# Kernel tuning notes

Measured on AMD Instinct MI355X. Metric: run time of the kernel, lower is better.

## Reference

```python
import jax, jax.numpy as jnp
import numpy as np

N_NODES = 50000
N_EDGES = 800000
IN_FEAT = 128
HEADS = 4
UNITS = 16
LEAKY_ALPHA = 0.2  # tf.nn.leaky_relu default


def setup_inputs() -> dict:
    key = jax.random.key(0)
    k1, k2, k3, k4, k5 = jax.random.split(key, 5)
    x = jax.random.normal(k1, (N_NODES, IN_FEAT), dtype=jnp.float32)
    edge_index = jax.random.randint(k2, (N_EDGES, 2), 0, N_NODES, dtype=jnp.int32)
    # Dense kernel (glorot-ish scaling), no bias (use_bias=False)
    W = jax.random.normal(k3, (IN_FEAT, HEADS * UNITS), dtype=jnp.float32) * (1.0 / np.sqrt(IN_FEAT))
    glorot = np.sqrt(2.0 / (1 + UNITS)).astype(np.float32)
    att_w1 = jax.random.normal(k4, (HEADS, 1, UNITS), dtype=jnp.float32) * glorot
    att_w2 = jax.random.normal(k5, (HEADS, 1, UNITS), dtype=jnp.float32) * glorot
    return {"x": x, "edge_index": edge_index, "W": W, "att_w1": att_w1, "att_w2": att_w2}


def reference(x, edge_index, W, att_w1, att_w2):
    n_nodes = x.shape[0]
    h = x @ W  # [N, H*U]
    snd_idx = edge_index[:, 0]
    rcv_idx = edge_index[:, 1]
    # gather per-edge features, split into heads -> [H, E, U]
    sender = h[snd_idx].reshape(-1, HEADS, UNITS).transpose(1, 0, 2)
    receiver = h[rcv_idx].reshape(-1, HEADS, UNITS).transpose(1, 0, 2)
    # per-edge, per-head attention logits [H, E]
    att = jnp.sum(att_w1 * sender, axis=-1) + jnp.sum(att_w2 * receiver, axis=-1)
    att = jnp.where(att > 0, att, LEAKY_ALPHA * att)
    # segment softmax over receiver neighborhoods, per head
    seg_max = jax.vmap(lambda a: jax.ops.segment_max(a, rcv_idx, num_segments=n_nodes))(att)  # [H, N]
    e = jnp.exp(att - seg_max[:, rcv_idx])
    denom = jax.vmap(lambda a: jax.ops.segment_sum(a, rcv_idx, num_segments=n_nodes))(e)  # [H, N]
    alpha = e / denom[:, rcv_idx]  # [H, E]
    # weighted scatter-sum of sender features -> [H, N, U]
    out = jax.vmap(lambda v: jax.ops.segment_sum(v, rcv_idx, num_segments=n_nodes))(sender * alpha[:, :, None])
    # concat heads -> [N, H*U]; activation is None (identity)
    return out.transpose(1, 0, 2).reshape(n_nodes, HEADS * UNITS)
```

## Files before the change

kernel.cpp:

```cpp
#include <hip/hip_runtime.h>
#include <math.h>

#define N_NODES 50000
#define N_EDGES 800000
#define IN_FEAT 128
#define HEADS   4
#define UNITS   16
#define OUTF    64
#define LEAKY   0.2f

#define NB      196
#define BCAP    5120
#define CAP     64
#define GEMM_BLKS 782
#define A_BLOCKS  196
#define EPB     16

typedef __attribute__((ext_vector_type(8))) short bf16x8;
typedef __attribute__((ext_vector_type(4))) float f32x4;

__device__ __forceinline__ unsigned short f2bf(float f) {
    unsigned u = __float_as_uint(f);
    unsigned r = u + 0x7FFFu + ((u >> 16) & 1u);
    return (unsigned short)(r >> 16);
}
__device__ __forceinline__ float bf2f(unsigned short b) {
    return __uint_as_float(((unsigned)b) << 16);
}

union SharedU {
    struct { unsigned short wt[64 * 136]; } g;
    struct { unsigned stage[4096]; int hist[256], cur[256], adj[256], wsum[4]; } a;
};

__global__ __launch_bounds__(256) void prep(const float* __restrict__ W,
                                            const float* __restrict__ w1,
                                            const float* __restrict__ w2,
                                            unsigned short* __restrict__ Wt_g,
                                            unsigned short* __restrict__ Wea_g,
                                            int* __restrict__ bucket_cnt) {
    int idx = blockIdx.x * 256 + threadIdx.x;
    if (idx < NB) bucket_cnt[idx] = 0;
    if (idx < IN_FEAT * OUTF) {
        int k = idx >> 6, c = idx & 63;
        Wt_g[c * IN_FEAT + k] = f2bf(W[idx]);
    }
    if (idx < IN_FEAT * HEADS) {
        int k = idx >> 2, hd = idx & 3;
        float s1 = 0.f, s2 = 0.f;
        #pragma unroll
        for (int u = 0; u < UNITS; ++u) {
            float wv = W[k * OUTF + hd * UNITS + u];
            s1 += wv * w1[hd * UNITS + u];
            s2 += wv * w2[hd * UNITS + u];
        }
        unsigned short h1 = f2bf(s1), h2 = f2bf(s2);
        unsigned short l1 = f2bf(s1 - bf2f(h1)), l2 = f2bf(s2 - bf2f(h2));
        Wea_g[(hd)      * IN_FEAT + k] = h1;
        Wea_g[(4 + hd)  * IN_FEAT + k] = h2;
        Wea_g[(8 + hd)  * IN_FEAT + k] = l1;
        Wea_g[(12 + hd) * IN_FEAT + k] = l2;
    }
}

__global__ __launch_bounds__(256, 8) void fused_gemm_bucketA(const float* __restrict__ x,
                                                             const unsigned short* __restrict__ Wt_g,
                                                             const unsigned short* __restrict__ Wea_g,
                                                             const int2* __restrict__ ei,
                                                             unsigned short* __restrict__ hg,
                                                             float* __restrict__ a1,
                                                             float* __restrict__ a2,
                                                             int* __restrict__ bucket_cnt,
                                                             unsigned* __restrict__ buckets) {
    __shared__ SharedU sh;
    const int t = threadIdx.x;
    const int lane = t & 63, wv = t >> 6;

    if (blockIdx.x >= GEMM_BLKS) {
        const int e0 = (blockIdx.x - GEMM_BLKS) * 4096;
        sh.a.hist[t] = 0;
        __syncthreads();

        unsigned pk[EPB]; int bk[EPB];
        #pragma unroll
        for (int j = 0; j < EPB; ++j) {
            int e = e0 + t + j * 256;
            if (e < N_EDGES) {
                int2 ed = ei[e];
                pk[j] = ((unsigned)ed.x << 16) | (unsigned)ed.y;
                bk[j] = ed.y >> 8;
                atomicAdd(&sh.a.hist[bk[j]], 1);
            } else bk[j] = -1;
        }
        __syncthreads();
        const int v = sh.a.hist[t];
        int inc = v;
        #pragma unroll
        for (int off = 1; off < 64; off <<= 1) {
            int u = __shfl_up(inc, off, 64);
            if (lane >= off) inc += u;
        }
        if (lane == 63) sh.a.wsum[wv] = inc;
        __syncthreads();
        const int s0 = sh.a.wsum[0], s1 = sh.a.wsum[1], s2 = sh.a.wsum[2];
        const int wo = (wv > 0 ? s0 : 0) + (wv > 1 ? s1 : 0) + (wv > 2 ? s2 : 0);
        const int excl = wo + inc - v;
        sh.a.cur[t] = excl;
        if (t < NB) {
            int g0 = atomicAdd(&bucket_cnt[t], v);
            sh.a.adj[t] = g0 - excl;
        }
        __syncthreads();
        #pragma unroll
        for (int j = 0; j < EPB; ++j) {
            if (bk[j] >= 0) {
                int p = atomicAdd(&sh.a.cur[bk[j]], 1);
                sh.a.stage[p] = pk[j];
            }
        }
        __syncthreads();
        const int total = min(4096, N_EDGES - e0);
        for (int i = t; i < total; i += 256) {
            unsigned vv = sh.a.stage[i];
            int b = (vv >> 8) & 255;
            buckets[(size_t)(b * BCAP + sh.a.adj[b] + i)] = vv;
        }
        return;
    }

    const int node0 = blockIdx.x * 64;
    unsigned short* wt = sh.g.wt;

    {
        const ushort4* Wt4 = (const ushort4*)Wt_g;
        #pragma unroll
        for (int it = 0; it < 8; ++it) {
            int idx = t + 256 * it;
            int c = idx >> 5, u = idx & 31;
            *(ushort4*)&wt[c * 136 + u * 4] = Wt4[idx];
        }
    }
    __syncthreads();

    const int m = lane & 15, quad = lane >> 4;
    const int n0 = wv * 16;
    const int arow = min(node0 + n0 + m, N_NODES - 1);
    const float* xr = x + (size_t)arow * IN_FEAT;

    f32x4 acc[4] = {{0,0,0,0},{0,0,0,0},{0,0,0,0},{0,0,0,0}};
    f32x4 acca   = {0,0,0,0};
    #pragma unroll
    for (int kc = 0; kc < 4; ++kc) {
        float4 v0 = *(const float4*)(xr + kc * 32 + quad * 8);
        float4 v1 = *(const float4*)(xr + kc * 32 + quad * 8 + 4);
        bf16x8 af;
        af[0] = (short)f2bf(v0.x); af[1] = (short)f2bf(v0.y);
        af[2] = (short)f2bf(v0.z); af[3] = (short)f2bf(v0.w);
        af[4] = (short)f2bf(v1.x); af[5] = (short)f2bf(v1.y);
        af[6] = (short)f2bf(v1.z); af[7] = (short)f2bf(v1.w);
        #pragma unroll
        for (int ct = 0; ct < 4; ++ct) {
            bf16x8 bfr = *(bf16x8*)&wt[(ct * 16 + m) * 136 + kc * 32 + quad * 8];
            acc[ct] = __builtin_amdgcn_mfma_f32_16x16x32_bf16(af, bfr, acc[ct], 0, 0, 0);
        }
        bf16x8 waf = *(const bf16x8*)(Wea_g + (size_t)m * IN_FEAT + kc * 32 + quad * 8);
        acca = __builtin_amdgcn_mfma_f32_16x16x32_bf16(af, waf, acca, 0, 0, 0);
    }

    #pragma unroll
    for (int r = 0; r < 4; ++r) {
        float vres = acca[r] + __shfl_xor(acca[r], 8, 64);
        int node = node0 + n0 + quad * 4 + r;
        if (node < N_NODES) {
            if (m < 4)      a1[node * 4 + m]       = vres;
            else if (m < 8) a2[node * 4 + (m - 4)] = vres;
        }
    }

    __syncthreads();
    unsigned short* hl = sh.g.wt;
    #pragma unroll
    for (int ct = 0; ct < 4; ++ct)
        #pragma unroll
        for (int r = 0; r < 4; ++r)
            hl[(n0 + quad * 4 + r) * 72 + ct * 16 + m] = f2bf(acc[ct][r]);
    __syncthreads();
    #pragma unroll
    for (int it = 0; it < 2; ++it) {
        int u = t + 256 * it;
        int r = u >> 3, cg = u & 7;
        int node = node0 + r;
        if (node < N_NODES)
            *(uint4*)&hg[(size_t)node * OUTF + cg * 8] = *(uint4*)&hl[r * 72 + cg * 8];
    }
}

__global__ __launch_bounds__(1024) void bucketB(const unsigned* __restrict__ buckets,
                                                const int* __restrict__ bucket_cnt,
                                                unsigned short* __restrict__ csr,
                                                int* __restrict__ deg) {
    __shared__ unsigned short snds[BCAP];
    __shared__ int hist[256], cur[256], strt[256], wsum[4];
    const int b = blockIdx.x;
    const int t = threadIdx.x;
    const int cnt = bucket_cnt[b];
    if (t < 256) hist[t] = 0;
    __syncthreads();
    for (int i = t; i < cnt; i += 1024)
        atomicAdd(&hist[buckets[(size_t)b * BCAP + i] & 255], 1);
    __syncthreads();
    int v = 0, inc = 0;
    if (t < 256) {
        const int lane = t & 63, wvx = t >> 6;
        v = hist[t];
        inc = v;
        #pragma unroll
        for (int off = 1; off < 64; off <<= 1) {
            int u = __shfl_up(inc, off, 64);
            if (lane >= off) inc += u;
        }
        if (lane == 63) wsum[wvx] = inc;
    }
    __syncthreads();
    if (t < 256) {
        const int wvx = t >> 6;
        const int s0 = wsum[0], s1 = wsum[1], s2 = wsum[2];
        const int wo = (wvx > 0 ? s0 : 0) + (wvx > 1 ? s1 : 0) + (wvx > 2 ? s2 : 0);
        const int excl = wo + inc - v;
        strt[t] = excl;
        cur[t]  = excl;
        const int node = b * 256 + t;
        if (node < N_NODES) deg[node] = v;
    }
    __syncthreads();
    for (int i = t; i < cnt; i += 1024) {
        unsigned vv = buckets[(size_t)b * BCAP + i];
        int p = atomicAdd(&cur[vv & 255], 1);
        snds[p] = (unsigned short)(vv >> 16);
    }
    __syncthreads();
    for (int u = t; u < 256 * CAP; u += 1024) {
        const int loc = u >> 6, slot = u & (CAP - 1);
        const int d = hist[loc];
        const unsigned short val = (d > 0) ? snds[strt[loc] + min(slot, d - 1)] : 0;
        csr[(size_t)b * (256 * CAP) + u] = val;
    }
}

__global__ __launch_bounds__(256, 8) void gather_kernel(const int* __restrict__ deg,
                                                        const unsigned short* __restrict__ csr,
                                                        const float* __restrict__ a1,
                                                        const float* __restrict__ a2,
                                                        const unsigned short* __restrict__ h,
                                                        float* __restrict__ out) {
    const int wave = threadIdx.x >> 6;
    const int lane = threadIdx.x & 63;
    const int n = blockIdx.x * 4 + wave;
    if (n >= N_NODES) return;
    const int sv = csr[(size_t)n * CAP + lane];
    const int cn = min(deg[n], CAP);
    const int sub  = lane >> 3;
    const int li   = lane & 7;
    const int head = li >> 1;
    if (cn <= 0) {
        if (sub == 0) {
            *(float4*)(out + (size_t)n * OUTF + li * 8)     = make_float4(0.f, 0.f, 0.f, 0.f);
            *(float4*)(out + (size_t)n * OUTF + li * 8 + 4) = make_float4(0.f, 0.f, 0.f, 0.f);
        }
        return;
    }
    const float a2h = a2[n * 4 + head];
    const uint4* h4 = (const uint4*)h;

    float acc[8] = {0.f,0.f,0.f,0.f,0.f,0.f,0.f,0.f};
    float den = 0.f;

    for (int i0 = 0; i0 < cn; i0 += 16) {
        #pragma unroll
        for (int g = 0; g < 2; ++g) {
            int er = i0 + g * 8 + sub;
            int ec = min(er, cn - 1);
            int s = __shfl(sv, ec, 64);
            float t0 = a1[s * 4 + head] + a2h;
            t0 = t0 > 0.f ? t0 : LEAKY * t0;
            float e = (er < cn) ? __expf(t0) : 0.f;
            uint4 hv = h4[(unsigned)(s * 8 + li)];
            const unsigned hw[4] = {hv.x, hv.y, hv.z, hv.w};
            #pragma unroll
            for (int q = 0; q < 4; ++q) {
                acc[q*2+0] = fmaf(e, __uint_as_float(hw[q] << 16),         acc[q*2+0]);
                acc[q*2+1] = fmaf(e, __uint_as_float(hw[q] & 0xFFFF0000u), acc[q*2+1]);
            }
            den += e;
        }
    }

    #pragma unroll
    for (int off = 8; off <= 32; off <<= 1) {
        #pragma unroll
        for (int q = 0; q < 8; ++q) acc[q] += __shfl_xor(acc[q], off, 64);
        den += __shfl_xor(den, off, 64);
    }

    if (sub == 0) {
        float inv = 1.f / den;
        *(float4*)(out + (size_t)n * OUTF + li * 8) =
            make_float4(acc[0] * inv, acc[1] * inv, acc[2] * inv, acc[3] * inv);
        *(float4*)(out + (size_t)n * OUTF + li * 8 + 4) =
            make_float4(acc[4] * inv, acc[5] * inv, acc[6] * inv, acc[7] * inv);
    }
}

extern "C" void kernel_launch(void* const* d_in, const int* in_sizes, int n_in,
                              void* d_out, int out_size, void* d_ws, size_t ws_size,
                              hipStream_t stream) {
    const float* x  = (const float*)d_in[0];
    const int2*  ei = (const int2*)d_in[1];
    const float* W  = (const float*)d_in[2];
    const float* w1 = (const float*)d_in[3];
    const float* w2 = (const float*)d_in[4];
    float* out = (float*)d_out;

    unsigned short* h    = (unsigned short*)d_ws;
    float* a1            = (float*)(h + (size_t)N_NODES * OUTF);
    float* a2            = a1 + (size_t)N_NODES * HEADS;
    unsigned short* Wt_g = (unsigned short*)(a2 + (size_t)N_NODES * HEADS);
    unsigned short* Wea_g = Wt_g + IN_FEAT * OUTF;
    int*   bucket_cnt    = (int*)(Wea_g + IN_FEAT * 16);
    unsigned* buckets    = (unsigned*)(bucket_cnt + 256);
    unsigned short* csr  = (unsigned short*)(buckets + (size_t)NB * BCAP);
    int*   deg           = (int*)(csr + (size_t)NB * 256 * CAP);

    prep<<<32, 256, 0, stream>>>(W, w1, w2, Wt_g, Wea_g, bucket_cnt);
    fused_gemm_bucketA<<<GEMM_BLKS + A_BLOCKS, 256, 0, stream>>>(x, Wt_g, Wea_g, ei,
                                                                 h, a1, a2,
                                                                 bucket_cnt, buckets);
    bucketB<<<NB, 1024, 0, stream>>>(buckets, bucket_cnt, csr, deg);
    gather_kernel<<<(N_NODES + 3) / 4, 256, 0, stream>>>(deg, csr, a1, a2, h, out);
}
```

Measured before the change: 125.8 us.

## Replace CSR build and per-node gather with bucket-local LDS atomic aggregation

Shrinks the receiver buckets to 64 nodes each and removes the second bucketing pass, the padded CSR and the per-node gather kernel. A new kernel walks each bucket's edges and accumulates exp-weighted sender features and denominators into shared memory with float atomics, using a rotated column layout to spread bank conflicts, then normalizes and writes out. This drops one kernel launch and the CSR write and read traffic, and also removes the 64-neighbor cap. In exchange it relies on shared-memory atomic throughput, skips the max subtraction, and makes the summation order nondeterministic.

```diff
diff --git a/kernel.cpp b/kernel.cpp
--- a/kernel.cpp
+++ b/kernel.cpp
@@ -9,12 +9,12 @@
 #define OUTF    64
 #define LEAKY   0.2f
 
-#define NB      196
-#define BCAP    5120
-#define CAP     64
+#define NB      782
+#define NBP     1024
+#define BCAP    1280
 #define GEMM_BLKS 782
-#define A_BLOCKS  196
-#define EPB     16
+#define A_BLOCKS  391
+#define EPB     8
 
 typedef __attribute__((ext_vector_type(8))) short bf16x8;
 typedef __attribute__((ext_vector_type(4))) float f32x4;
@@ -30,7 +30,8 @@
 
 union SharedU {
     struct { unsigned short wt[64 * 136]; } g;
-    struct { unsigned stage[4096]; int hist[256], cur[256], adj[256], wsum[4]; } a;
+    struct { unsigned stage[2048]; int hist[NBP], cur[NBP];
+             short adj[NBP]; int wsum[4]; } a;
 };
 
 __global__ __launch_bounds__(256) void prep(const float* __restrict__ W,
@@ -40,7 +41,7 @@
                                             unsigned short* __restrict__ Wea_g,
                                             int* __restrict__ bucket_cnt) {
     int idx = blockIdx.x * 256 + threadIdx.x;
-    if (idx < NB) bucket_cnt[idx] = 0;
+    if (idx < NBP) bucket_cnt[idx] = 0;
     if (idx < IN_FEAT * OUTF) {
         int k = idx >> 6, c = idx & 63;
         Wt_g[c * IN_FEAT + k] = f2bf(W[idx]);
@@ -77,8 +78,9 @@
     const int lane = t & 63, wv = t >> 6;
 
     if (blockIdx.x >= GEMM_BLKS) {
-        const int e0 = (blockIdx.x - GEMM_BLKS) * 4096;
-        sh.a.hist[t] = 0;
+        const int e0 = (blockIdx.x - GEMM_BLKS) * 2048;
+        #pragma unroll
+        for (int j = 0; j < 4; ++j) sh.a.hist[t + 256 * j] = 0;
         __syncthreads();
 
         unsigned pk[EPB]; int bk[EPB];
@@ -88,13 +90,15 @@
             if (e < N_EDGES) {
                 int2 ed = ei[e];
                 pk[j] = ((unsigned)ed.x << 16) | (unsigned)ed.y;
-                bk[j] = ed.y >> 8;
+                bk[j] = ed.y >> 6;
                 atomicAdd(&sh.a.hist[bk[j]], 1);
             } else bk[j] = -1;
         }
         __syncthreads();
-        const int v = sh.a.hist[t];
-        int inc = v;
+        const int h0 = sh.a.hist[4 * t + 0], h1 = sh.a.hist[4 * t + 1],
+                  h2 = sh.a.hist[4 * t + 2], h3 = sh.a.hist[4 * t + 3];
+        const int lsum = h0 + h1 + h2 + h3;
+        int inc = lsum;
         #pragma unroll
         for (int off = 1; off < 64; off <<= 1) {
             int u = __shfl_up(inc, off, 64);
@@ -104,11 +108,16 @@
         __syncthreads();
         const int s0 = sh.a.wsum[0], s1 = sh.a.wsum[1], s2 = sh.a.wsum[2];
         const int wo = (wv > 0 ? s0 : 0) + (wv > 1 ? s1 : 0) + (wv > 2 ? s2 : 0);
-        const int excl = wo + inc - v;
-        sh.a.cur[t] = excl;
-        if (t < NB) {
-            int g0 = atomicAdd(&bucket_cnt[t], v);
-            sh.a.adj[t] = g0 - excl;
+        const int base = wo + inc - lsum;
+        const int ex[4] = { base, base + h0, base + h0 + h1, base + h0 + h1 + h2 };
+        const int hh[4] = { h0, h1, h2, h3 };
+        #pragma unroll
+        for (int j = 0; j < 4; ++j) {
+            sh.a.cur[4 * t + j] = ex[j];
+            if (4 * t + j < NB) {
+                int g0 = atomicAdd(&bucket_cnt[4 * t + j], hh[j]);
+                sh.a.adj[4 * t + j] = (short)(g0 - ex[j]);
+            } else sh.a.adj[4 * t + j] = 0;
         }
         __syncthreads();
         #pragma unroll
@@ -119,11 +128,11 @@
             }
         }
         __syncthreads();
-        const int total = min(4096, N_EDGES - e0);
+        const int total = min(2048, N_EDGES - e0);
         for (int i = t; i < total; i += 256) {
             unsigned vv = sh.a.stage[i];
-            int b = (vv >> 8) & 255;
-            buckets[(size_t)(b * BCAP + sh.a.adj[b] + i)] = vv;
+            int b = (vv & 0xFFFFu) >> 6;
+            buckets[(size_t)(b * BCAP + (int)sh.a.adj[b] + i)] = vv;
         }
         return;
     }
@@ -195,119 +204,60 @@
     }
 }
 
-__global__ __launch_bounds__(1024) void bucketB(const unsigned* __restrict__ buckets,
-                                                const int* __restrict__ bucket_cnt,
-                                                unsigned short* __restrict__ csr,
-                                                int* __restrict__ deg) {
-    __shared__ unsigned short snds[BCAP];
-    __shared__ int hist[256], cur[256], strt[256], wsum[4];
+__global__ __launch_bounds__(512, 8) void edge_aggregate(const unsigned* __restrict__ buckets,
+                                                         const int* __restrict__ bucket_cnt,
+                                                         const float* __restrict__ a1,
+                                                         const float* __restrict__ a2,
+                                                         const unsigned short* __restrict__ h,
+                                                         float* __restrict__ out) {
+    __shared__ float acc[64 * OUTF];
+    __shared__ float den[64 * HEADS];
     const int b = blockIdx.x;
     const int t = threadIdx.x;
     const int cnt = bucket_cnt[b];
-    if (t < 256) hist[t] = 0;
-    __syncthreads();
-    for (int i = t; i < cnt; i += 1024)
-        atomicAdd(&hist[buckets[(size_t)b * BCAP + i] & 255], 1);
-    __syncthreads();
-    int v = 0, inc = 0;
+
+    for (int u = t; u < 64 * OUTF; u += 512) acc[u] = 0.f;
+    if (t < 256) den[t] = 0.f;
+    __syncthreads();
+
+    const int g    = t >> 3;
+    const int li   = t & 7;
+    const int head = li >> 1;
+    const uint4* h4 = (const uint4*)h;
+
+    for (int i = g; i < cnt; i += 64) {
+        unsigned v = buckets[(size_t)b * BCAP + i];
+        const int snd = v >> 16;
+        const int rcv = v & 0xFFFF;
+        const int loc = rcv & 63;
+        float t0 = a1[snd * 4 + head] + a2[rcv * 4 + head];
+        t0 = t0 > 0.f ? t0 : LEAKY * t0;
+        const float e = __expf(t0);
+        uint4 hv = h4[(unsigned)snd * 8 + li];
+        const unsigned hw[4] = {hv.x, hv.y, hv.z, hv.w};
+        float* arow = &acc[loc * OUTF];
+        const int cb = li * 8 + loc * 8;
+        #pragma unroll
+        for (int q = 0; q < 4; ++q) {
+            unsafeAtomicAdd(&arow[(cb + 2 * q)     & 63], e * __uint_as_float(hw[q] << 16));
+            unsafeAtomicAdd(&arow[(cb + 2 * q + 1) & 63], e * __uint_as_float(hw[q] & 0xFFFF0000u));
+        }
+        if (!(li & 1)) unsafeAtomicAdd(&den[loc * 4 + head], e);
+    }
+    __syncthreads();
+
     if (t < 256) {
-        const int lane = t & 63, wvx = t >> 6;
-        v = hist[t];
-        inc = v;
-        #pragma unroll
-        for (int off = 1; off < 64; off <<= 1) {
-            int u = __shfl_up(inc, off, 64);
-            if (lane >= off) inc += u;
-        }
-        if (lane == 63) wsum[wvx] = inc;
-    }
-    __syncthreads();
-    if (t < 256) {
-        const int wvx = t >> 6;
-        const int s0 = wsum[0], s1 = wsum[1], s2 = wsum[2];
-        const int wo = (wvx > 0 ? s0 : 0) + (wvx > 1 ? s1 : 0) + (wvx > 2 ? s2 : 0);
-        const int excl = wo + inc - v;
-        strt[t] = excl;
-        cur[t]  = excl;
-        const int node = b * 256 + t;
-        if (node < N_NODES) deg[node] = v;
-    }
-    __syncthreads();
-    for (int i = t; i < cnt; i += 1024) {
-        unsigned vv = buckets[(size_t)b * BCAP + i];
-        int p = atomicAdd(&cur[vv & 255], 1);
-        snds[p] = (unsigned short)(vv >> 16);
-    }
-    __syncthreads();
-    for (int u = t; u < 256 * CAP; u += 1024) {
-        const int loc = u >> 6, slot = u & (CAP - 1);
-        const int d = hist[loc];
-        const unsigned short val = (d > 0) ? snds[strt[loc] + min(slot, d - 1)] : 0;
-        csr[(size_t)b * (256 * CAP) + u] = val;
-    }
-}
-
-__global__ __launch_bounds__(256, 8) void gather_kernel(const int* __restrict__ deg,
-                                                        const unsigned short* __restrict__ csr,
-                                                        const float* __restrict__ a1,
-                                                        const float* __restrict__ a2,
-                                                        const unsigned short* __restrict__ h,
-                                                        float* __restrict__ out) {
-    const int wave = threadIdx.x >> 6;
-    const int lane = threadIdx.x & 63;
-    const int n = blockIdx.x * 4 + wave;
-    if (n >= N_NODES) return;
-    const int sv = csr[(size_t)n * CAP + lane];
-    const int cn = min(deg[n], CAP);
-    const int sub  = lane >> 3;
-    const int li   = lane & 7;
-    const int head = li >> 1;
-    if (cn <= 0) {
-        if (sub == 0) {
-            *(float4*)(out + (size_t)n * OUTF + li * 8)     = make_float4(0.f, 0.f, 0.f, 0.f);
-            *(float4*)(out + (size_t)n * OUTF + li * 8 + 4) = make_float4(0.f, 0.f, 0.f, 0.f);
-        }
-        return;
-    }
-    const float a2h = a2[n * 4 + head];
-    const uint4* h4 = (const uint4*)h;
-
-    float acc[8] = {0.f,0.f,0.f,0.f,0.f,0.f,0.f,0.f};
-    float den = 0.f;
-
-    for (int i0 = 0; i0 < cn; i0 += 16) {
-        #pragma unroll
-        for (int g = 0; g < 2; ++g) {
-            int er = i0 + g * 8 + sub;
-            int ec = min(er, cn - 1);
-            int s = __shfl(sv, ec, 64);
-            float t0 = a1[s * 4 + head] + a2h;
-            t0 = t0 > 0.f ? t0 : LEAKY * t0;
-            float e = (er < cn) ? __expf(t0) : 0.f;
-            uint4 hv = h4[(unsigned)(s * 8 + li)];
-            const unsigned hw[4] = {hv.x, hv.y, hv.z, hv.w};
-            #pragma unroll
-            for (int q = 0; q < 4; ++q) {
-                acc[q*2+0] = fmaf(e, __uint_as_float(hw[q] << 16),         acc[q*2+0]);
-                acc[q*2+1] = fmaf(e, __uint_as_float(hw[q] & 0xFFFF0000u), acc[q*2+1]);
-            }
-            den += e;
-        }
-    }
-
-    #pragma unroll
-    for (int off = 8; off <= 32; off <<= 1) {
-        #pragma unroll
-        for (int q = 0; q < 8; ++q) acc[q] += __shfl_xor(acc[q], off, 64);
-        den += __shfl_xor(den, off, 64);
-    }
-
-    if (sub == 0) {
-        float inv = 1.f / den;
-        *(float4*)(out + (size_t)n * OUTF + li * 8) =
-            make_float4(acc[0] * inv, acc[1] * inv, acc[2] * inv, acc[3] * inv);
-        *(float4*)(out + (size_t)n * OUTF + li * 8 + 4) =
-            make_float4(acc[4] * inv, acc[5] * inv, acc[6] * inv, acc[7] * inv);
+        float d = den[t];
+        den[t] = (d > 0.f) ? 1.f / d : 0.f;
+    }
+    __syncthreads();
+
+    for (int u = t; u < 64 * OUTF; u += 512) {
+        const int loc = u >> 6, col = u & 63;
+        const int node = b * 64 + loc;
+        if (node < N_NODES)
+            out[(size_t)node * OUTF + col] =
+                acc[loc * OUTF + ((col + loc * 8) & 63)] * den[loc * 4 + (col >> 4)];
     }
 }
 
@@ -327,14 +277,11 @@
     unsigned short* Wt_g = (unsigned short*)(a2 + (size_t)N_NODES * HEADS);
     unsigned short* Wea_g = Wt_g + IN_FEAT * OUTF;
     int*   bucket_cnt    = (int*)(Wea_g + IN_FEAT * 16);
-    unsigned* buckets    = (unsigned*)(bucket_cnt + 256);
-    unsigned short* csr  = (unsigned short*)(buckets + (size_t)NB * BCAP);
-    int*   deg           = (int*)(csr + (size_t)NB * 256 * CAP);
+    unsigned* buckets    = (unsigned*)(bucket_cnt + NBP);
 
     prep<<<32, 256, 0, stream>>>(W, w1, w2, Wt_g, Wea_g, bucket_cnt);
     fused_gemm_bucketA<<<GEMM_BLKS + A_BLOCKS, 256, 0, stream>>>(x, Wt_g, Wea_g, ei,
                                                                  h, a1, a2,
                                                                  bucket_cnt, buckets);
-    bucketB<<<NB, 1024, 0, stream>>>(buckets, bucket_cnt, csr, deg);
-    gather_kernel<<<(N_NODES + 3) / 4, 256, 0, stream>>>(deg, csr, a1, a2, h, out);
-}
+    edge_aggregate<<<NB, 512, 0, stream>>>(buckets, bucket_cnt, a1, a2, h, out);
+}
```

Result: slower. 475.1 us (+277.7%).
